# Kernel optimization log

Measured on AMD Instinct MI355X. Metric: run time of the kernel, lower is better.

## Reference

```python
import jax, jax.numpy as jnp
import numpy as np

DIM = 1024
NUM_HEADS = 16
HEAD_DIM = DIM // NUM_HEADS
SCALE = HEAD_DIM ** -0.5


def rotate_half(x):
    x1, x2 = jnp.split(x, 2, axis=-1)
    return jnp.concatenate((-x2, x1), axis=-1)


def setup_inputs() -> dict:
    key = jax.random.key(0)
    ks = jax.random.split(key, 8)
    B, N = 2, 2048
    x = jax.random.normal(ks[0], (B, N, DIM), dtype=jnp.float32)
    # RoPE tables, broadcast over batch and heads
    pos = jnp.arange(N, dtype=jnp.float32)[:, None]
    inv_freq = 1.0 / (10000.0 ** (jnp.arange(0, HEAD_DIM, 2, dtype=jnp.float32) / HEAD_DIM))
    ang = pos * inv_freq[None, :]                       # [N, HEAD_DIM/2]
    ang = jnp.concatenate([ang, ang], axis=-1)          # [N, HEAD_DIM]
    rope_cos = jnp.cos(ang)[None, None]                 # [1,1,N,HEAD_DIM]
    rope_sin = jnp.sin(ang)[None, None]
    s = DIM ** -0.5
    qkv_w = jax.random.normal(ks[1], (3 * DIM, DIM), dtype=jnp.float32) * s
    qkv_b = jnp.zeros((3 * DIM,), dtype=jnp.float32)
    proj_w = jax.random.normal(ks[2], (DIM, DIM), dtype=jnp.float32) * s
    proj_b = jnp.zeros((DIM,), dtype=jnp.float32)
    return {"x": x, "rope_cos": rope_cos, "rope_sin": rope_sin,
            "qkv_w": qkv_w, "qkv_b": qkv_b, "proj_w": proj_w, "proj_b": proj_b}


def reference(x, rope_cos, rope_sin, qkv_w, qkv_b, proj_w, proj_b):
    B, N, C = x.shape
    H, D = NUM_HEADS, HEAD_DIM
    qkv = x @ qkv_w.T + qkv_b                            # [B,N,3C]
    qkv = qkv.reshape(B, N, 3, H, D).transpose(2, 0, 3, 1, 4)  # [3,B,H,N,D]
    q, k, v = qkv[0], qkv[1], qkv[2]
    # RoPE on q, k
    q = q * rope_cos + rotate_half(q) * rope_sin
    k = k * rope_cos + rotate_half(k) * rope_sin
    # scaled dot-product attention
    scores = jnp.einsum('bhnd,bhmd->bhnm', q, k) * SCALE
    attn = jax.nn.softmax(scores, axis=-1)
    out = jnp.einsum('bhnm,bhmd->bhnd', attn, v)         # [B,H,N,D]
    out = out.transpose(0, 2, 1, 3).reshape(B, N, C)
    return out @ proj_w.T + proj_b
```

## Files before the change

kernel.cpp:

```cpp
#include <hip/hip_runtime.h>
#include <hip/hip_bf16.h>

#define NUM_HEADS 16
#define HEAD_DIM 64
#define DIM 1024
#define NTOK 2048
#define MTOT 4096

typedef __attribute__((ext_vector_type(8))) short bf16x8;
typedef __attribute__((ext_vector_type(4))) float f32x4;
typedef __attribute__((ext_vector_type(16))) float f32x16;
typedef __attribute__((ext_vector_type(2))) unsigned int uint2v;

__device__ __forceinline__ unsigned short f2bf(float f) {
    union { __hip_bfloat16 h; unsigned short u; } c;
    c.h = __float2bfloat16(f);
    return c.u;
}

__device__ __forceinline__ unsigned int packbf(float lo, float hi) {
    union { unsigned short us[2]; unsigned int u; } p;
    p.us[0] = f2bf(lo); p.us[1] = f2bf(hi);
    return p.u;
}

__device__ __forceinline__ void plswap(unsigned int &a, unsigned int &b) {
#if __has_builtin(__builtin_amdgcn_permlane32_swap)
    uint2v r = __builtin_amdgcn_permlane32_swap(a, b, false, false);
    a = r[0]; b = r[1];
#else
    unsigned int pa = (unsigned int)__shfl_xor((int)a, 32);
    unsigned int pb = (unsigned int)__shfl_xor((int)b, 32);
    bool hi = (threadIdx.x & 32) != 0;
    unsigned int an = hi ? pb : a;
    unsigned int bn = hi ? b : pa;
    a = an; b = bn;
#endif
}

__device__ __forceinline__ void gload16(const unsigned short* g, unsigned short* l) {
    __builtin_amdgcn_global_load_lds(
        (const __attribute__((address_space(1))) void*)g,
        (__attribute__((address_space(3))) void*)l, 16, 0, 0);
}

__global__ __launch_bounds__(256) void k_conv3(
    const float* __restrict__ s0, unsigned short* __restrict__ d0, int n0,
    const float* __restrict__ s1, unsigned short* __restrict__ d1, int n1,
    const float* __restrict__ s2, unsigned short* __restrict__ d2, int n2)
{
    int blk = blockIdx.x;
    int b0 = n0 >> 11, b1 = n1 >> 11;
    const float* s; unsigned short* d; int i;
    if (blk < b0)            { s = s0; d = d0; i = blk; }
    else if (blk < b0 + b1)  { s = s1; d = d1; i = blk - b0; }
    else                     { s = s2; d = d2; i = blk - b0 - b1; }
    int idx = (i * 256 + threadIdx.x) * 8;
    float4 a = *(const float4*)(s + idx);
    float4 b = *(const float4*)(s + idx + 4);
    union { unsigned short us[8]; uint4 u4; } p;
    p.us[0] = f2bf(a.x); p.us[1] = f2bf(a.y); p.us[2] = f2bf(a.z); p.us[3] = f2bf(a.w);
    p.us[4] = f2bf(b.x); p.us[5] = f2bf(b.y); p.us[6] = f2bf(b.z); p.us[7] = f2bf(b.w);
    *(uint4*)(d + idx) = p.u4;
}

__global__ __launch_bounds__(256) void k_gemm_qkv(
    const unsigned short* __restrict__ xb, const unsigned short* __restrict__ wb,
    const float* __restrict__ bias, const float* __restrict__ rcos,
    const float* __restrict__ rsin,
    unsigned short* __restrict__ qb, unsigned short* __restrict__ kb,
    unsigned short* __restrict__ vtb)
{
    __shared__ __align__(16) unsigned char smem[34816];
    unsigned short* As = (unsigned short*)smem;
    unsigned short* Bs = (unsigned short*)(smem + 16384);

    const int tid  = threadIdx.x;
    const int lane = tid & 63;
    const int wid  = tid >> 6;
    const int lc   = lane & 31;
    const int hi   = lane >> 5;
    const int wm   = (wid >> 1) * 64;
    const int wn   = (wid & 1) * 64;
    const int m0   = blockIdx.y * 128;
    const int n0   = blockIdx.x * 128;

    const f32x16 z16 = {0.f,0.f,0.f,0.f, 0.f,0.f,0.f,0.f, 0.f,0.f,0.f,0.f, 0.f,0.f,0.f,0.f};
    f32x16 acc[2][2];
    acc[0][0] = z16; acc[0][1] = z16; acc[1][0] = z16; acc[1][1] = z16;

    for (int k0 = 0; k0 < DIM; k0 += 64) {
        #pragma unroll
        for (int it = 0; it < 4; ++it) {
            int p   = tid + it * 256;
            int row = p >> 3;
            int c   = (p & 7) ^ (row & 7);
            gload16(xb + (size_t)(m0 + row) * DIM + k0 + c*8, As + p*8);
            gload16(wb + (size_t)(n0 + row) * DIM + k0 + c*8, Bs + p*8);
        }
        __syncthreads();
        #pragma unroll
        for (int kk = 0; kk < 4; ++kk) {
            bf16x8 af[2], bfr[2];
            #pragma unroll
            for (int i = 0; i < 2; ++i) {
                int row = wm + i*32 + lc;
                af[i] = *(const bf16x8*)(As + row*64 + (((kk*2 + hi) ^ (row & 7)) << 3));
            }
            #pragma unroll
            for (int j = 0; j < 2; ++j) {
                int row = wn + j*32 + lc;
                bfr[j] = *(const bf16x8*)(Bs + row*64 + (((kk*2 + hi) ^ (row & 7)) << 3));
            }
            #pragma unroll
            for (int i = 0; i < 2; ++i)
                #pragma unroll
                for (int j = 0; j < 2; ++j)
                    acc[i][j] = __builtin_amdgcn_mfma_f32_32x32x16_bf16(af[i], bfr[j], acc[i][j], 0, 0, 0);
        }
        __syncthreads();
    }

    const int sect = n0 >> 10;
    float bq[2];
    #pragma unroll
    for (int j = 0; j < 2; ++j) bq[j] = bias[n0 + wn + j*32 + lc];

    if (sect < 2) {
        unsigned short* dst = sect ? kb : qb;
        const float sc = sect ? 1.0f : 0.125f * 1.44269504088896f;
        const int h = ((n0 & 1023) + wn) >> 6;
        #pragma unroll
        for (int i = 0; i < 2; ++i) {
            #pragma unroll
            for (int r = 0; r < 16; ++r) {
                int gm = m0 + wm + i*32 + (r & 3) + 8*(r >> 2) + 4*hi;
                int b  = gm >> 11, n = gm & 2047;
                size_t base = ((size_t)(b*NUM_HEADS + h) * NTOK + n) << 6;
                #pragma unroll
                for (int j = 0; j < 2; ++j) {
                    int d = j*32 + lc;
                    float val = acc[i][j][r] + bq[j];
                    float vp  = acc[i][j^1][r] + bq[j^1];
                    float rot = (j == 0) ? -vp : vp;
                    float c = rcos[n*64 + d], s = rsin[n*64 + d];
                    dst[base + d] = f2bf((val * c + rot * s) * sc);
                }
            }
        }
    } else {
        unsigned short (*vt)[136] = (unsigned short (*)[136])smem;
        __syncthreads();
        #pragma unroll
        for (int i = 0; i < 2; ++i)
            #pragma unroll
            for (int j = 0; j < 2; ++j)
                #pragma unroll
                for (int r = 0; r < 16; ++r) {
                    int row = wm + i*32 + (r & 3) + 8*(r >> 2) + 4*hi;
                    int c   = wn + j*32 + lc;
                    vt[c][row] = f2bf(acc[i][j][r] + bq[j]);
                }
        __syncthreads();
        const int b = m0 >> 11;
        const int nbase = m0 & 2047;
        #pragma unroll
        for (int it = 0; it < 8; ++it) {
            int c   = (tid >> 4) + it * 16;
            int sc2 = (n0 & 1023) + c;
            int hh  = sc2 >> 6, d = sc2 & 63;
            int nloc = (tid & 15) * 8;
            uint4 val = *(uint4*)&vt[c][nloc];
            *(uint4*)(vtb + ((size_t)(b*NUM_HEADS + hh) * HEAD_DIM + d) * NTOK + nbase + nloc) = val;
        }
    }
}

__global__ __launch_bounds__(256, 2) void k_attn(
    const unsigned short* __restrict__ qb, const unsigned short* __restrict__ kb,
    const unsigned short* __restrict__ vtb, unsigned short* __restrict__ attnb)
{
    __shared__ __align__(16) char sb[65536];

    const int tid  = threadIdx.x;
    const int lane = tid & 63;
    const int w    = tid >> 6;
    const int hi   = lane >> 5;
    const int lc   = lane & 31;
    const int qg   = w >> 1;
    const int kvg  = w & 1;
    const int q0   = blockIdx.y * 128;
    const int bh   = blockIdx.x;
    const int b    = bh >> 4, h = bh & 15;

    int koff[2][4];
    #pragma unroll
    for (int s = 0; s < 2; ++s)
        #pragma unroll
        for (int ks = 0; ks < 4; ++ks)
            koff[s][ks] = (64*kvg + 32*s + lc) * 128 + (((2*ks + hi) ^ (lc & 7)) << 4);
    int voff[2][4];
    #pragma unroll
    for (int dt = 0; dt < 2; ++dt)
        #pragma unroll
        for (int c4 = 0; c4 < 4; ++c4)
            voff[dt][c4] = 32768 + (32*dt + lc) * 256 + (((8*kvg + 2*c4 + hi) ^ (lc & 15)) << 4);

    const unsigned short* gk[4];
    const unsigned short* gv[4];
    char* dk[4]; char* dv[4];
    {
        const unsigned short* kbase = kb  + (size_t)bh * NTOK * 64;
        const unsigned short* vbase = vtb + (size_t)bh * HEAD_DIM * NTOK;
        #pragma unroll
        for (int it = 0; it < 4; ++it) {
            int p  = tid + it * 256;
            int kr = p >> 3;
            int kc = (p & 7) ^ (kr & 7);
            gk[it] = kbase + kr*64 + kc*8;
            dk[it] = sb + p*16;
            int vr = p >> 4;
            int vc = (p & 15) ^ (vr & 15);
            gv[it] = vbase + (size_t)vr*NTOK + vc*8;
            dv[it] = sb + 32768 + p*16;
        }
    }

    bf16x8 qa[2][4];
    #pragma unroll
    for (int qt = 0; qt < 2; ++qt) {
        size_t qrow = ((size_t)bh * NTOK + q0 + 64*qg + 32*qt + lc) * 64;
        #pragma unroll
        for (int ks = 0; ks < 4; ++ks)
            qa[qt][ks] = *(const bf16x8*)(qb + qrow + ks*16 + hi*8);
    }

    const f32x16 z16 = {0.f,0.f,0.f,0.f, 0.f,0.f,0.f,0.f, 0.f,0.f,0.f,0.f, 0.f,0.f,0.f,0.f};
    f32x16 o2[2][2];
    o2[0][0] = z16; o2[0][1] = z16; o2[1][0] = z16; o2[1][1] = z16;
    float lsum0 = 0.f, lsum1 = 0.f;

    #pragma unroll
    for (int it = 0; it < 4; ++it) {
        gload16(gk[it], (unsigned short*)dk[it]);
        gload16(gv[it], (unsigned short*)dv[it]);
        gk[it] += 8192; gv[it] += 128;
    }
    __syncthreads();

#define SUM16(SS) ( (((SS[0]+SS[1])+(SS[2]+SS[3])) + ((SS[4]+SS[5])+(SS[6]+SS[7]))) + \
                    (((SS[8]+SS[9])+(SS[10]+SS[11])) + ((SS[12]+SS[13])+(SS[14]+SS[15]))) )

#define PACKQT(SS, PB0, PB1)                                                     \
    {                                                                            \
        _Pragma("unroll")                                                        \
        for (int u = 0; u < 2; ++u) {                                            \
            unsigned int a0 = packbf(SS[8*u],     SS[8*u + 1]);                  \
            unsigned int b0 = packbf(SS[8*u + 4], SS[8*u + 5]);                  \
            unsigned int a1 = packbf(SS[8*u + 2], SS[8*u + 3]);                  \
            unsigned int b1 = packbf(SS[8*u + 6], SS[8*u + 7]);                  \
            plswap(a0, b0);                                                      \
            plswap(a1, b1);                                                      \
            union { unsigned int u4[4]; bf16x8 v; } pk;                          \
            pk.u4[0] = a0; pk.u4[1] = a1; pk.u4[2] = b0; pk.u4[3] = b1;          \
            if (u == 0) (PB0) = pk.v; else (PB1) = pk.v;                         \
        }                                                                        \
    }

#define ATTN_ITER(X, DO_STAGE)                                                   \
    {                                                                            \
        if (DO_STAGE) {                                                          \
            _Pragma("unroll")                                                    \
            for (int it = 0; it < 4; ++it) {                                     \
                gload16(gk[it], (unsigned short*)(dk[it] + ((X) ^ 16384)));      \
                gload16(gv[it], (unsigned short*)(dv[it] + ((X) ^ 16384)));      \
                gk[it] += 8192; gv[it] += 128;                                   \
            }                                                                    \
        }                                                                        \
        _Pragma("unroll")                                                        \
        for (int s = 0; s < 2; ++s) {                                            \
            bf16x8 kf[4];                                                        \
            _Pragma("unroll")                                                    \
            for (int ks = 0; ks < 4; ++ks)                                       \
                kf[ks] = *(const bf16x8*)(sb + (X) + koff[s][ks]);               \
            __builtin_amdgcn_s_setprio(1);                                       \
            f32x16 S0 = __builtin_amdgcn_mfma_f32_32x32x16_bf16(kf[0], qa[0][0], z16, 0, 0, 0); \
            f32x16 S1 = __builtin_amdgcn_mfma_f32_32x32x16_bf16(kf[0], qa[1][0], z16, 0, 0, 0); \
            _Pragma("unroll")                                                    \
            for (int ks = 1; ks < 4; ++ks) {                                     \
                S0 = __builtin_amdgcn_mfma_f32_32x32x16_bf16(kf[ks], qa[0][ks], S0, 0, 0, 0); \
                S1 = __builtin_amdgcn_mfma_f32_32x32x16_bf16(kf[ks], qa[1][ks], S1, 0, 0, 0); \
            }                                                                    \
            __builtin_amdgcn_s_setprio(0);                                       \
            _Pragma("unroll")                                                    \
            for (int r = 0; r < 16; ++r) {                                       \
                S0[r] = __builtin_amdgcn_exp2f(S0[r]);                           \
                S1[r] = __builtin_amdgcn_exp2f(S1[r]);                           \
            }                                                                    \
            lsum0 += SUM16(S0);                                                  \
            lsum1 += SUM16(S1);                                                  \
            bf16x8 p00, p01, p10, p11;                                           \
            PACKQT(S0, p00, p01);                                                \
            PACKQT(S1, p10, p11);                                                \
            _Pragma("unroll")                                                    \
            for (int u = 0; u < 2; ++u) {                                        \
                bf16x8 pb0 = u ? p01 : p00;                                      \
                bf16x8 pb1 = u ? p11 : p10;                                      \
                _Pragma("unroll")                                                \
                for (int dt = 0; dt < 2; ++dt) {                                 \
                    bf16x8 vf = *(const bf16x8*)(sb + (X) + voff[dt][2*s + u]);  \
                    __builtin_amdgcn_s_setprio(1);                               \
                    o2[0][dt] = __builtin_amdgcn_mfma_f32_32x32x16_bf16(vf, pb0, o2[0][dt], 0, 0, 0); \
                    o2[1][dt] = __builtin_amdgcn_mfma_f32_32x32x16_bf16(vf, pb1, o2[1][dt], 0, 0, 0); \
                    __builtin_amdgcn_s_setprio(0);                               \
                }                                                                \
            }                                                                    \
        }                                                                        \
        __syncthreads();                                                         \
    }

    #pragma unroll 1
    for (int tt = 0; tt < NTOK/128; tt += 2) {
        ATTN_ITER(0,     true);
        ATTN_ITER(16384, (tt + 2 < NTOK/128));
    }
#undef ATTN_ITER
#undef PACKQT
#undef SUM16

    lsum0 += __shfl_xor(lsum0, 32);
    lsum1 += __shfl_xor(lsum1, 32);

    if (kvg == 1) {
        char* base = sb + qg * 16384;
        #pragma unroll
        for (int qt = 0; qt < 2; ++qt)
            #pragma unroll
            for (int dt = 0; dt < 2; ++dt)
                #pragma unroll
                for (int part = 0; part < 4; ++part) {
                    f32x4 v4;
                    #pragma unroll
                    for (int v = 0; v < 4; ++v) v4[v] = o2[qt][dt][part*4 + v];
                    *(f32x4*)(base + ((qt*2 + dt)*4 + part)*1024 + lane*16) = v4;
                }
        *(float*)(sb + 32768 + (qg*2 + 0)*256 + lane*4) = lsum0;
        *(float*)(sb + 32768 + (qg*2 + 1)*256 + lane*4) = lsum1;
    }
    __syncthreads();
    if (kvg == 0) {
        char* base = sb + qg * 16384;
        float lp0 = *(const float*)(sb + 32768 + (qg*2 + 0)*256 + lane*4);
        float lp1 = *(const float*)(sb + 32768 + (qg*2 + 1)*256 + lane*4);
        const float inv0 = 1.0f / (lsum0 + lp0);
        const float inv1 = 1.0f / (lsum1 + lp1);
        #pragma unroll
        for (int qt = 0; qt < 2; ++qt) {
            const float inv = qt ? inv1 : inv0;
            int q = q0 + 64*qg + 32*qt + lc;
            size_t obase = ((size_t)(b*NTOK + q)) * DIM + h*HEAD_DIM;
            #pragma unroll
            for (int dt = 0; dt < 2; ++dt)
                #pragma unroll
                for (int c = 0; c < 4; ++c) {
                    f32x4 vp = *(const f32x4*)(base + ((qt*2 + dt)*4 + c)*1024 + lane*16);
                    union { unsigned short us[4]; uint2 u2; } pk4;
                    #pragma unroll
                    for (int v = 0; v < 4; ++v)
                        pk4.us[v] = f2bf((o2[qt][dt][c*4 + v] + vp[v]) * inv);
                    *(uint2*)(attnb + obase + dt*32 + 8*c + 4*hi) = pk4.u2;
                }
        }
    }
}

__global__ __launch_bounds__(256) void k_proj(
    const unsigned short* __restrict__ a, const unsigned short* __restrict__ wb,
    const float* __restrict__ bias, float* __restrict__ out)
{
    __shared__ __align__(16) unsigned short As[8192];
    __shared__ __align__(16) unsigned short Bs[4096];

    const int tid  = threadIdx.x;
    const int lane = tid & 63;
    const int wid  = tid >> 6;
    const int lc   = lane & 31;
    const int hi   = lane >> 5;
    const int wm   = (wid & 1) * 64;
    const int wn   = (wid >> 1) * 32;
    const int m0   = blockIdx.y * 128;
    const int n0   = blockIdx.x * 64;

    const f32x16 z16 = {0.f,0.f,0.f,0.f, 0.f,0.f,0.f,0.f, 0.f,0.f,0.f,0.f, 0.f,0.f,0.f,0.f};
    f32x16 acc[2];
    acc[0] = z16; acc[1] = z16;

    for (int k0 = 0; k0 < DIM; k0 += 64) {
        #pragma unroll
        for (int it = 0; it < 4; ++it) {
            int p   = tid + it * 256;
            int row = p >> 3;
            int c   = (p & 7) ^ (row & 7);
            gload16(a + (size_t)(m0 + row) * DIM + k0 + c*8, As + p*8);
        }
        #pragma unroll
        for (int it = 0; it < 2; ++it) {
            int p   = tid + it * 256;
            int row = p >> 3;
            int c   = (p & 7) ^ (row & 7);
            gload16(wb + (size_t)(n0 + row) * DIM + k0 + c*8, Bs + p*8);
        }
        __syncthreads();
        #pragma unroll
        for (int kk = 0; kk < 4; ++kk) {
            bf16x8 af[2], bf;
            #pragma unroll
            for (int i = 0; i < 2; ++i) {
                int row = wm + i*32 + lc;
                af[i] = *(const bf16x8*)(As + row*64 + (((kk*2 + hi) ^ (row & 7)) << 3));
            }
            {
                int row = wn + lc;
                bf = *(const bf16x8*)(Bs + row*64 + (((kk*2 + hi) ^ (row & 7)) << 3));
            }
            #pragma unroll
            for (int i = 0; i < 2; ++i)
                acc[i] = __builtin_amdgcn_mfma_f32_32x32x16_bf16(af[i], bf, acc[i], 0, 0, 0);
        }
        __syncthreads();
    }

    #pragma unroll
    for (int i = 0; i < 2; ++i)
        #pragma unroll
        for (int r = 0; r < 16; ++r) {
            int row = m0 + wm + i*32 + (r & 3) + 8*(r >> 2) + 4*hi;
            int col = n0 + wn + lc;
            out[(size_t)row * DIM + col] = acc[i][r] + bias[col];
        }
}

extern "C" void kernel_launch(void* const* d_in, const int* in_sizes, int n_in,
                              void* d_out, int out_size, void* d_ws, size_t ws_size,
                              hipStream_t stream)
{
    const float* x      = (const float*)d_in[0];
    const float* rcos   = (const float*)d_in[1];
    const float* rsin   = (const float*)d_in[2];
    const float* qkv_w  = (const float*)d_in[3];
    const float* qkv_b  = (const float*)d_in[4];
    const float* proj_w = (const float*)d_in[5];
    const float* proj_b = (const float*)d_in[6];
    float* out = (float*)d_out;

    const size_t BUF = (size_t)2 * NUM_HEADS * NTOK * HEAD_DIM;
    unsigned short* qb    = (unsigned short*)d_ws;
    unsigned short* kb    = qb + BUF;
    unsigned short* vtb   = kb + BUF;
    unsigned short* attnb = vtb + BUF;
    unsigned short* xbf   = attnb + BUF;
    unsigned short* wqkvb = xbf + (size_t)MTOT * DIM;
    unsigned short* wprjb = wqkvb + (size_t)3 * DIM * DIM;

    const int n0 = MTOT * DIM, n1 = 3 * DIM * DIM, n2 = DIM * DIM;
    k_conv3<<<dim3((n0 + n1 + n2) / 2048), 256, 0, stream>>>(
        x, xbf, n0, qkv_w, wqkvb, n1, proj_w, wprjb, n2);

    k_gemm_qkv<<<dim3(24, 32), 256, 0, stream>>>(xbf, wqkvb, qkv_b, rcos, rsin, qb, kb, vtb);
    k_attn<<<dim3(32, NTOK/128), 256, 0, stream>>>(qb, kb, vtb, attnb);
    k_proj<<<dim3(16, 32), 256, 0, stream>>>(attnb, wprjb, proj_b, out);
}
```

Before: 115.7 us.

## Single-buffer K/V tiles in attention to halve LDS and raise occupancy

The attention kernel drops its double-buffered K/V LDS staging. It now loads each 128-token tile into one buffer, waits on a barrier, computes, and barriers again. This cuts shared memory from 64KB to about 33KB so more blocks can be resident per CU, at the cost of no longer overlapping global-to-LDS loads with MFMA work inside a block. The row-sum reduction is also rewritten as a vector-halving sum.

```diff
diff --git a/kernel.cpp b/kernel.cpp
--- a/kernel.cpp
+++ b/kernel.cpp
@@ -9,6 +9,7 @@
 
 typedef __attribute__((ext_vector_type(8))) short bf16x8;
 typedef __attribute__((ext_vector_type(4))) float f32x4;
+typedef __attribute__((ext_vector_type(8))) float f32x8;
 typedef __attribute__((ext_vector_type(16))) float f32x16;
 typedef __attribute__((ext_vector_type(2))) unsigned int uint2v;
 
@@ -36,6 +37,15 @@
     unsigned int bn = hi ? b : pa;
     a = an; b = bn;
 #endif
+}
+
+__device__ __forceinline__ float sum16v(f32x16 S) {
+    f32x8 lo = __builtin_shufflevector(S, S, 0, 1, 2, 3, 4, 5, 6, 7);
+    f32x8 hi = __builtin_shufflevector(S, S, 8, 9, 10, 11, 12, 13, 14, 15);
+    f32x8 s8 = lo + hi;
+    f32x4 a4 = __builtin_shufflevector(s8, s8, 0, 1, 2, 3) +
+               __builtin_shufflevector(s8, s8, 4, 5, 6, 7);
+    return (a4[0] + a4[1]) + (a4[2] + a4[3]);
 }
 
 __device__ __forceinline__ void gload16(const unsigned short* g, unsigned short* l) {
@@ -180,7 +190,7 @@
     const unsigned short* __restrict__ qb, const unsigned short* __restrict__ kb,
     const unsigned short* __restrict__ vtb, unsigned short* __restrict__ attnb)
 {
-    __shared__ __align__(16) char sb[65536];
+    __shared__ __align__(16) char sb[33792];
 
     const int tid  = threadIdx.x;
     const int lane = tid & 63;
@@ -204,7 +214,7 @@
     for (int dt = 0; dt < 2; ++dt)
         #pragma unroll
         for (int c4 = 0; c4 < 4; ++c4)
-            voff[dt][c4] = 32768 + (32*dt + lc) * 256 + (((8*kvg + 2*c4 + hi) ^ (lc & 15)) << 4);
+            voff[dt][c4] = 16384 + (32*dt + lc) * 256 + (((8*kvg + 2*c4 + hi) ^ (lc & 15)) << 4);
 
     const unsigned short* gk[4];
     const unsigned short* gv[4];
@@ -222,7 +232,7 @@
             int vr = p >> 4;
             int vc = (p & 15) ^ (vr & 15);
             gv[it] = vbase + (size_t)vr*NTOK + vc*8;
-            dv[it] = sb + 32768 + p*16;
+            dv[it] = sb + 16384 + p*16;
         }
     }
 
@@ -239,17 +249,6 @@
     f32x16 o2[2][2];
     o2[0][0] = z16; o2[0][1] = z16; o2[1][0] = z16; o2[1][1] = z16;
     float lsum0 = 0.f, lsum1 = 0.f;
-
-    #pragma unroll
-    for (int it = 0; it < 4; ++it) {
-        gload16(gk[it], (unsigned short*)dk[it]);
-        gload16(gv[it], (unsigned short*)dv[it]);
-        gk[it] += 8192; gv[it] += 128;
-    }
-    __syncthreads();
-
-#define SUM16(SS) ( (((SS[0]+SS[1])+(SS[2]+SS[3])) + ((SS[4]+SS[5])+(SS[6]+SS[7]))) + \
-                    (((SS[8]+SS[9])+(SS[10]+SS[11])) + ((SS[12]+SS[13])+(SS[14]+SS[15]))) )
 
 #define PACKQT(SS, PB0, PB1)                                                     \
     {                                                                            \
@@ -267,66 +266,58 @@
         }                                                                        \
     }
 
-#define ATTN_ITER(X, DO_STAGE)                                                   \
-    {                                                                            \
-        if (DO_STAGE) {                                                          \
-            _Pragma("unroll")                                                    \
-            for (int it = 0; it < 4; ++it) {                                     \
-                gload16(gk[it], (unsigned short*)(dk[it] + ((X) ^ 16384)));      \
-                gload16(gv[it], (unsigned short*)(dv[it] + ((X) ^ 16384)));      \
-                gk[it] += 8192; gv[it] += 128;                                   \
-            }                                                                    \
-        }                                                                        \
-        _Pragma("unroll")                                                        \
-        for (int s = 0; s < 2; ++s) {                                            \
-            bf16x8 kf[4];                                                        \
-            _Pragma("unroll")                                                    \
-            for (int ks = 0; ks < 4; ++ks)                                       \
-                kf[ks] = *(const bf16x8*)(sb + (X) + koff[s][ks]);               \
-            __builtin_amdgcn_s_setprio(1);                                       \
-            f32x16 S0 = __builtin_amdgcn_mfma_f32_32x32x16_bf16(kf[0], qa[0][0], z16, 0, 0, 0); \
-            f32x16 S1 = __builtin_amdgcn_mfma_f32_32x32x16_bf16(kf[0], qa[1][0], z16, 0, 0, 0); \
-            _Pragma("unroll")                                                    \
-            for (int ks = 1; ks < 4; ++ks) {                                     \
-                S0 = __builtin_amdgcn_mfma_f32_32x32x16_bf16(kf[ks], qa[0][ks], S0, 0, 0, 0); \
-                S1 = __builtin_amdgcn_mfma_f32_32x32x16_bf16(kf[ks], qa[1][ks], S1, 0, 0, 0); \
-            }                                                                    \
-            __builtin_amdgcn_s_setprio(0);                                       \
-            _Pragma("unroll")                                                    \
-            for (int r = 0; r < 16; ++r) {                                       \
-                S0[r] = __builtin_amdgcn_exp2f(S0[r]);                           \
-                S1[r] = __builtin_amdgcn_exp2f(S1[r]);                           \
-            }                                                                    \
-            lsum0 += SUM16(S0);                                                  \
-            lsum1 += SUM16(S1);                                                  \
-            bf16x8 p00, p01, p10, p11;                                           \
-            PACKQT(S0, p00, p01);                                                \
-            PACKQT(S1, p10, p11);                                                \
-            _Pragma("unroll")                                                    \
-            for (int u = 0; u < 2; ++u) {                                        \
-                bf16x8 pb0 = u ? p01 : p00;                                      \
-                bf16x8 pb1 = u ? p11 : p10;                                      \
-                _Pragma("unroll")                                                \
-                for (int dt = 0; dt < 2; ++dt) {                                 \
-                    bf16x8 vf = *(const bf16x8*)(sb + (X) + voff[dt][2*s + u]);  \
-                    __builtin_amdgcn_s_setprio(1);                               \
-                    o2[0][dt] = __builtin_amdgcn_mfma_f32_32x32x16_bf16(vf, pb0, o2[0][dt], 0, 0, 0); \
-                    o2[1][dt] = __builtin_amdgcn_mfma_f32_32x32x16_bf16(vf, pb1, o2[1][dt], 0, 0, 0); \
-                    __builtin_amdgcn_s_setprio(0);                               \
-                }                                                                \
-            }                                                                    \
-        }                                                                        \
-        __syncthreads();                                                         \
-    }
-
     #pragma unroll 1
-    for (int tt = 0; tt < NTOK/128; tt += 2) {
-        ATTN_ITER(0,     true);
-        ATTN_ITER(16384, (tt + 2 < NTOK/128));
-    }
-#undef ATTN_ITER
+    for (int t = 0; t < NTOK/128; ++t) {
+        #pragma unroll
+        for (int it = 0; it < 4; ++it) {
+            gload16(gk[it], (unsigned short*)dk[it]);
+            gload16(gv[it], (unsigned short*)dv[it]);
+            gk[it] += 8192; gv[it] += 128;
+        }
+        __syncthreads();
+
+        #pragma unroll
+        for (int s = 0; s < 2; ++s) {
+            bf16x8 kf[4];
+            #pragma unroll
+            for (int ks = 0; ks < 4; ++ks)
+                kf[ks] = *(const bf16x8*)(sb + koff[s][ks]);
+            __builtin_amdgcn_s_setprio(1);
+            f32x16 S0 = __builtin_amdgcn_mfma_f32_32x32x16_bf16(kf[0], qa[0][0], z16, 0, 0, 0);
+            f32x16 S1 = __builtin_amdgcn_mfma_f32_32x32x16_bf16(kf[0], qa[1][0], z16, 0, 0, 0);
+            #pragma unroll
+            for (int ks = 1; ks < 4; ++ks) {
+                S0 = __builtin_amdgcn_mfma_f32_32x32x16_bf16(kf[ks], qa[0][ks], S0, 0, 0, 0);
+                S1 = __builtin_amdgcn_mfma_f32_32x32x16_bf16(kf[ks], qa[1][ks], S1, 0, 0, 0);
+            }
+            __builtin_amdgcn_s_setprio(0);
+            #pragma unroll
+            for (int r = 0; r < 16; ++r) {
+                S0[r] = __builtin_amdgcn_exp2f(S0[r]);
+                S1[r] = __builtin_amdgcn_exp2f(S1[r]);
+            }
+            lsum0 += sum16v(S0);
+            lsum1 += sum16v(S1);
+            bf16x8 p00, p01, p10, p11;
+            PACKQT(S0, p00, p01);
+            PACKQT(S1, p10, p11);
+            #pragma unroll
+            for (int u = 0; u < 2; ++u) {
+                bf16x8 pb0 = u ? p01 : p00;
+                bf16x8 pb1 = u ? p11 : p10;
+                #pragma unroll
+                for (int dt = 0; dt < 2; ++dt) {
+                    bf16x8 vf = *(const bf16x8*)(sb + voff[dt][2*s + u]);
+                    __builtin_amdgcn_s_setprio(1);
+                    o2[0][dt] = __builtin_amdgcn_mfma_f32_32x32x16_bf16(vf, pb0, o2[0][dt], 0, 0, 0);
+                    o2[1][dt] = __builtin_amdgcn_mfma_f32_32x32x16_bf16(vf, pb1, o2[1][dt], 0, 0, 0);
+                    __builtin_amdgcn_s_setprio(0);
+                }
+            }
+        }
+        __syncthreads();
+    }
 #undef PACKQT
-#undef SUM16
 
     lsum0 += __shfl_xor(lsum0, 32);
     lsum1 += __shfl_xor(lsum1, 32);
```

Result: slower. 120.3 us (+4.0%).
